# Performance work log

Measured on AMD Instinct MI355X. Metric: run time of the kernel, lower is better.

Reference implementation:

```python
import jax, jax.numpy as jnp
import numpy as np


def _lstm_cell(x, h, c, w_ih, w_hh, b_ih, b_hh):
    # PyTorch LSTMCell gate order: i, f, g, o
    z = x @ w_ih.T + h @ w_hh.T + b_ih + b_hh
    i, f, g, o = jnp.split(z, 4, axis=-1)
    c_new = jax.nn.sigmoid(f) * c + jax.nn.sigmoid(i) * jnp.tanh(g)
    h_new = jax.nn.sigmoid(o) * jnp.tanh(c_new)
    return h_new, c_new


def setup_inputs() -> dict:
    B, T_in, T_out = 32, 512, 512
    n_mel, n_frames = 80, 1
    n_enc, n_att, n_filt, K = 512, 128, 32, 31
    n_arnn, n_drnn, n_pre = 1024, 1024, 256
    keys = jax.random.split(jax.random.key(0), 25)
    r = lambda k, *s: jax.random.normal(keys[k], s, dtype=jnp.float32) * 0.05
    return {
        "memory": jax.random.normal(keys[0], (B, T_in, n_enc), dtype=jnp.float32),
        "decoder_inputs": jax.random.normal(keys[1], (B, n_mel, T_out), dtype=jnp.float32),
        "memory_lengths": jax.random.randint(keys[2], (B,), T_in // 2, T_in + 1).astype(jnp.int32),
        "prenet_w1": r(3, n_pre, n_mel * n_frames),
        "prenet_w2": r(4, n_pre, n_pre),
        "arnn_w_ih": r(5, 4 * n_arnn, n_pre + n_enc),
        "arnn_w_hh": r(6, 4 * n_arnn, n_arnn),
        "arnn_b_ih": r(7, 4 * n_arnn),
        "arnn_b_hh": r(8, 4 * n_arnn),
        "query_w": r(9, n_att, n_arnn),
        "memory_w": r(10, n_att, n_enc),
        "v_w": r(11, 1, n_att),
        "loc_conv_w": r(12, n_filt, 2, K),
        "loc_dense_w": r(13, n_att, n_filt),
        "drnn_w_ih": r(14, 4 * n_drnn, n_arnn + n_enc),
        "drnn_w_hh": r(15, 4 * n_drnn, n_drnn),
        "drnn_b_ih": r(16, 4 * n_drnn),
        "drnn_b_hh": r(17, 4 * n_drnn),
        "proj_w": r(18, n_mel * n_frames, n_drnn + n_enc),
        "proj_b": r(19, n_mel * n_frames),
        "gate_w": r(20, 1, n_drnn + n_enc),
        "gate_b": r(21, 1),
    }


def reference(memory, decoder_inputs, memory_lengths, prenet_w1, prenet_w2,
              arnn_w_ih, arnn_w_hh, arnn_b_ih, arnn_b_hh,
              query_w, memory_w, v_w, loc_conv_w, loc_dense_w,
              drnn_w_ih, drnn_w_hh, drnn_b_ih, drnn_b_hh,
              proj_w, proj_b, gate_w, gate_b):
    B, T_in, n_enc = memory.shape
    n_mel, T_out = decoder_inputs.shape[1], decoder_inputs.shape[2]
    n_arnn = arnn_w_hh.shape[1]
    n_drnn = drnn_w_hh.shape[1]
    K = loc_conv_w.shape[-1]
    dt = memory.dtype

    # mask: True = padded position (masked_fill with -inf in torch)
    mask = jnp.arange(T_in)[None, :] >= memory_lengths[:, None]          # (B, T_in)
    processed_memory = memory @ memory_w.T                               # (B, T_in, n_att)

    # teacher-forced inputs with go frame: (T_out+1, B, n_mel)
    go = jnp.zeros((1, B, n_mel), dt)
    dec_in = jnp.concatenate([go, jnp.transpose(decoder_inputs, (2, 0, 1))], 0)
    # prenet (dropout omitted for a deterministic reference)
    pre = jax.nn.relu(dec_in @ prenet_w1.T)
    pre = jax.nn.relu(pre @ prenet_w2.T)[:-1]                            # (T_out, B, n_pre)

    init = (jnp.zeros((B, n_arnn), dt), jnp.zeros((B, n_arnn), dt),
            jnp.zeros((B, n_drnn), dt), jnp.zeros((B, n_drnn), dt),
            jnp.zeros((B, T_in), dt), jnp.zeros((B, T_in), dt),
            jnp.zeros((B, n_enc), dt))

    def step(carry, pre_t):
        ah, ac, dh, dc, aw, aw_cum, actx = carry
        # attention RNN
        ah, ac = _lstm_cell(jnp.concatenate([pre_t, actx], -1), ah, ac,
                            arnn_w_ih, arnn_w_hh, arnn_b_ih, arnn_b_hh)
        # location-sensitive attention
        aw_cat = jnp.stack([aw, aw_cum], axis=1)                         # (B, 2, T_in)
        loc = jax.lax.conv_general_dilated(
            aw_cat, loc_conv_w, (1,), [(K // 2, K // 2)],
            dimension_numbers=("NCH", "OIH", "NCH"))                   # (B, n_filt, T_in)
        loc = jnp.transpose(loc, (0, 2, 1)) @ loc_dense_w.T              # (B, T_in, n_att)
        pq = (ah @ query_w.T)[:, None, :]                                # (B, 1, n_att)
        e = (jnp.tanh(pq + loc + processed_memory) @ v_w.T)[..., 0]      # (B, T_in)
        e = jnp.where(mask, -jnp.inf, e)
        aw = jax.nn.softmax(e, axis=1)
        actx = jnp.einsum("bt,bte->be", aw, memory)                      # (B, n_enc)
        aw_cum = aw_cum + aw
        # decoder RNN
        dh, dc = _lstm_cell(jnp.concatenate([ah, actx], -1), dh, dc,
                            drnn_w_ih, drnn_w_hh, drnn_b_ih, drnn_b_hh)
        dhc = jnp.concatenate([dh, actx], -1)
        mel = dhc @ proj_w.T + proj_b
        gate = (dhc @ gate_w.T + gate_b)[:, 0]
        return (ah, ac, dh, dc, aw, aw_cum, actx), (mel, gate, aw)

    _, (mels, gates, aligns) = jax.lax.scan(step, init, pre)
    mel_outputs = jnp.transpose(mels, (1, 2, 0))        # (B, n_mel, T_out)
    gate_outputs = gates.T                              # (B, T_out)
    alignments = jnp.transpose(aligns, (1, 0, 2))       # (B, T_out, T_in)
    return mel_outputs, gate_outputs, alignments
```

## Files before the change

kernel.cpp:

```cpp
#include <hip/hip_runtime.h>
#include <math.h>

#define NB 32
#define TIN 512
#define TOUT 512
#define NENC 512
#define NATT 128
#define NU 1024
#define NG 4096
#define NPRE 256
#define NMEL 80

#define WS_AH    0u
#define WS_AC    32768u
#define WS_DH    65536u
#define WS_DC    98304u
#define WS_ACTX  131072u
#define WS_AW    147456u
#define WS_AWCUM 163840u
#define WS_E     180224u
#define WS_PQ    196608u
#define WS_FLG   200704u
#define WS_ZD    201728u
#define WS_ZA    2823168u
#define WS_PM    4658176u
#define WS_PRE   6755328u
#define WS_WBF   10957824u
#define WS_STATE_ZERO_BYTES (WS_ZD * 4u)
#define OUT_ALIGN ((size_t)NB * NMEL * TOUT + (size_t)NB * TOUT)

#define BW_DIH 0u
#define BW_DHH 6291456u
#define BW_AIH 10485760u
#define BW_AHH 13631488u

__device__ __forceinline__ float fsigm(float x) { return 1.f / (1.f + __expf(-x)); }
__device__ __forceinline__ float ftanh(float x) { return 1.f - 2.f / (__expf(2.f * x) + 1.f); }
__device__ __forceinline__ float bf2f(unsigned short h) { return __uint_as_float((unsigned)h << 16); }

__device__ __forceinline__ void st_wt(float* p, float v) {
    asm volatile("global_store_dword %0, %1, off sc0 sc1" :: "v"(p), "v"(v) : "memory");
}

__global__ __launch_bounds__(256) void packbf_kernel(const float* __restrict__ src,
                                                     unsigned short* __restrict__ dst, int n) {
    for (int i = blockIdx.x * 256 + threadIdx.x; i < n; i += gridDim.x * 256) {
        unsigned u = __float_as_uint(src[i]);
        dst[i] = (unsigned short)((u + 0x7FFFu + ((u >> 16) & 1u)) >> 16);
    }
}

__global__ __launch_bounds__(256) void prenet1_kernel(const float* __restrict__ dec,
                                                      const float* __restrict__ w1,
                                                      float* __restrict__ pre) {
    int t = blockIdx.x;
    __shared__ float xl[NB][NMEL];
    for (int i = threadIdx.x; i < NB * NMEL; i += 256) {
        int b = i / NMEL, m = i % NMEL;
        xl[b][m] = (t == 0) ? 0.0f : dec[(b * NMEL + m) * TOUT + (t - 1)];
    }
    __syncthreads();
    int j = threadIdx.x;
    float acc[NB];
#pragma unroll
    for (int b = 0; b < NB; b++) acc[b] = 0.0f;
    for (int m = 0; m < NMEL; m++) {
        float w = w1[j * NMEL + m];
#pragma unroll
        for (int b = 0; b < NB; b++) acc[b] += xl[b][m] * w;
    }
    for (int b = 0; b < NB; b++) pre[((size_t)t * NB + b) * NPRE + j] = fmaxf(acc[b], 0.0f);
}

__global__ __launch_bounds__(256) void prenet2_kernel(const float* __restrict__ w2,
                                                      float* __restrict__ pre) {
    int t = blockIdx.x;
    __shared__ float hl[NB][NPRE];
    for (int i = threadIdx.x; i < NB * NPRE; i += 256)
        hl[i / NPRE][i % NPRE] = pre[(size_t)t * NB * NPRE + i];
    __syncthreads();
    int j = threadIdx.x;
    float acc[NB];
#pragma unroll
    for (int b = 0; b < NB; b++) acc[b] = 0.0f;
    for (int k = 0; k < NPRE; k++) {
        float w = w2[j * NPRE + k];
#pragma unroll
        for (int b = 0; b < NB; b++) acc[b] += hl[b][k] * w;
    }
    for (int b = 0; b < NB; b++) pre[((size_t)t * NB + b) * NPRE + j] = fmaxf(acc[b], 0.0f);
}

__global__ __launch_bounds__(128) void pm_kernel(const float* __restrict__ mem,
                                                 const float* __restrict__ mw,
                                                 float* __restrict__ pm) {
    int b = blockIdx.y, t0 = blockIdx.x * 4;
    __shared__ float ml[4][NENC];
    for (int i = threadIdx.x; i < 4 * NENC; i += 128)
        ml[i / NENC][i % NENC] = mem[((size_t)b * TIN + t0 + i / NENC) * NENC + (i % NENC)];
    __syncthreads();
    int a = threadIdx.x;
    float acc[4] = {0, 0, 0, 0};
    for (int e = 0; e < NENC; e++) {
        float w = mw[a * NENC + e];
#pragma unroll
        for (int tt = 0; tt < 4; tt++) acc[tt] += ml[tt][e] * w;
    }
    for (int tt = 0; tt < 4; tt++)
        pm[((size_t)b * TIN + t0 + tt) * NATT + a] = acc[tt];
}

__global__ __launch_bounds__(256) void z_all_kernel(
        const unsigned short* __restrict__ wbf,
        const float* __restrict__ ws_base, const float* __restrict__ pre_t,
        float* __restrict__ zd, float* __restrict__ za) {
    int col = blockIdx.x * 256 + threadIdx.x;
    int s = blockIdx.y;
    const float* ah   = ws_base + WS_AH;
    const float* dh   = ws_base + WS_DH;
    const float* actx = ws_base + WS_ACTX;
    const unsigned short* W; const float* x; int xs;
    if (s < 8)       { W = wbf + BW_DIH + (size_t)col * 1536 + s * 128;              x = ah + s * 128;           xs = NU;   }
    else if (s < 12) { W = wbf + BW_DIH + (size_t)col * 1536 + 1024 + (s - 8) * 128; x = actx + (s - 8) * 128;   xs = NENC; }
    else if (s < 20) { W = wbf + BW_DHH + (size_t)col * 1024 + (s - 12) * 128;       x = dh + (s - 12) * 128;    xs = NU;   }
    else if (s < 22) { W = wbf + BW_AIH + (size_t)col * 768 + (s - 20) * 128;        x = pre_t + (s - 20) * 128; xs = NPRE; }
    else if (s < 26) { W = wbf + BW_AIH + (size_t)col * 768 + 256 + (s - 22) * 128;  x = actx + (s - 22) * 128;  xs = NENC; }
    else             { W = wbf + BW_AHH + (size_t)col * 1024 + (s - 26) * 128;       x = ah + (s - 26) * 128;    xs = NU;   }

    float acc[NB];
#pragma unroll
    for (int b = 0; b < NB; b++) acc[b] = 0.0f;
    for (int k4 = 0; k4 < 32; k4++) {
        ushort4 h4 = *(const ushort4*)(W + k4 * 4);
        float w0 = bf2f(h4.x), w1 = bf2f(h4.y), w2 = bf2f(h4.z), w3 = bf2f(h4.w);
#pragma unroll
        for (int b = 0; b < NB; b++) {
            float4 x4 = *(const float4*)(x + (size_t)b * xs + k4 * 4);
            acc[b] = fmaf(w0, x4.x, acc[b]);
            acc[b] = fmaf(w1, x4.y, acc[b]);
            acc[b] = fmaf(w2, x4.z, acc[b]);
            acc[b] = fmaf(w3, x4.w, acc[b]);
        }
    }
    float* zp = ((s < 20) ? (zd + (size_t)s * NB * NG) : (za + (size_t)(s - 20) * NB * NG)) + col;
#pragma unroll
    for (int b = 0; b < NB; b++) zp[(size_t)b * NG] = acc[b];
}

__global__ __launch_bounds__(256) void softmax_ctx_kernel(const float* __restrict__ mem,
                                                          const float* __restrict__ E,
                                                          float* __restrict__ AW,
                                                          float* __restrict__ AWCUM,
                                                          float* __restrict__ ACTX,
                                                          float* __restrict__ out_align, int step) {
    int b = blockIdx.y, ec = blockIdx.x;
    __shared__ float el[TIN];
    __shared__ float red[256];
    __shared__ float part[4][64];
    const float* Eb = E + b * TIN;
    for (int i = threadIdx.x; i < TIN; i += 256) el[i] = Eb[i];
    __syncthreads();
    red[threadIdx.x] = fmaxf(el[threadIdx.x], el[threadIdx.x + 256]);
    __syncthreads();
    for (int s = 128; s > 0; s >>= 1) {
        if (threadIdx.x < s) red[threadIdx.x] = fmaxf(red[threadIdx.x], red[threadIdx.x + s]);
        __syncthreads();
    }
    float mx = red[0];
    __syncthreads();
    float p0 = __expf(el[threadIdx.x] - mx), p1 = __expf(el[threadIdx.x + 256] - mx);
    el[threadIdx.x] = p0; el[threadIdx.x + 256] = p1;
    red[threadIdx.x] = p0 + p1;
    __syncthreads();
    for (int s = 128; s > 0; s >>= 1) {
        if (threadIdx.x < s) red[threadIdx.x] += red[threadIdx.x + s];
        __syncthreads();
    }
    float inv = 1.0f / red[0];
    int ei = ec * 64 + (threadIdx.x & 63), tp4 = threadIdx.x >> 6;
    float acc = 0.0f;
    const float* mb = mem + (size_t)b * TIN * NENC + ei;
    for (int t = tp4 * 128; t < tp4 * 128 + 128; t++) acc += el[t] * mb[(size_t)t * NENC];
    part[tp4][threadIdx.x & 63] = acc;
    __syncthreads();
    if (threadIdx.x < 64) {
        float ctx = (part[0][threadIdx.x] + part[1][threadIdx.x] +
                     part[2][threadIdx.x] + part[3][threadIdx.x]) * inv;
        ACTX[b * NENC + ec * 64 + threadIdx.x] = ctx;
    }
    if (ec == 0) {
        for (int i = threadIdx.x; i < TIN; i += 256) {
            float a_ = el[i] * inv;
            AW[b * TIN + i] = a_;
            AWCUM[b * TIN + i] += a_;
            out_align[((size_t)b * TOUT + step) * TIN + i] = a_;
        }
    }
}

__global__ __launch_bounds__(512) void ge_kernel(
        const float* __restrict__ abih, const float* __restrict__ abhh,
        const float* __restrict__ qw,
        const float* __restrict__ dbih, const float* __restrict__ dbhh,
        const float* __restrict__ pjw, const float* __restrict__ pjb,
        const float* __restrict__ gtw, const float* __restrict__ gtb,
        const float* __restrict__ wc, const float* __restrict__ ldw,
        const float* __restrict__ vw, const int* __restrict__ mlen,
        float* __restrict__ ws, float* __restrict__ out, int t) {
    __shared__ float sm[5888];
    int tid = threadIdx.x, bid = blockIdx.x;
    unsigned* flg = (unsigned*)(ws + WS_FLG) + (t + 1);

    if (bid < 32) {
        if (t < 0) return;
        int b = bid;
        float* DH = ws + WS_DH + (size_t)b * NU;
        float* DC = ws + WS_DC + (size_t)b * NU;
        for (int u = tid; u < NU; u += 512) {
            float zi = dbih[u]          + dbhh[u];
            float zf = dbih[NU + u]     + dbhh[NU + u];
            float zg = dbih[2 * NU + u] + dbhh[2 * NU + u];
            float zo = dbih[3 * NU + u] + dbhh[3 * NU + u];
            for (int s = 0; s < 20; s++) {
                const float* z = ws + WS_ZD + ((size_t)s * NB + b) * NG;
                zi += z[u]; zf += z[NU + u]; zg += z[2 * NU + u]; zo += z[3 * NU + u];
            }
            float c = fsigm(zf) * DC[u] + fsigm(zi) * ftanh(zg);
            float h = fsigm(zo) * ftanh(c);
            DC[u] = c; DH[u] = h; sm[u] = h;
        }
        for (int i = tid; i < NENC; i += 512) sm[NU + i] = ws[WS_ACTX + b * NENC + i];
        __syncthreads();
        int col = tid >> 2, q = tid & 3;
        if (col < 81) {
            const float* wr = (col < 80) ? (pjw + (size_t)col * 1536) : gtw;
            const float* d4 = sm + q * 384;
            const float* w4 = wr + q * 384;
            float s = 0.f;
#pragma unroll
            for (int k4 = 0; k4 < 96; k4++) {
                float4 hv = *(const float4*)(d4 + k4 * 4);
                float4 wv = *(const float4*)(w4 + k4 * 4);
                s = fmaf(hv.x, wv.x, s); s = fmaf(hv.y, wv.y, s);
                s = fmaf(hv.z, wv.z, s); s = fmaf(hv.w, wv.w, s);
            }
            s += __shfl_xor(s, 1); s += __shfl_xor(s, 2);
            if (q == 0) {
                s += (col < 80) ? pjb[col] : gtb[0];
                if (col < 80) out[((size_t)b * NMEL + col) * TOUT + t] = s;
                else          out[(size_t)NB * NMEL * TOUT + (size_t)b * TOUT + t] = s;
            }
        }
        return;
    }
    if (bid < 64) {
        if (t + 1 >= TOUT) return;
        int b = bid - 32;
        float* AH = ws + WS_AH + (size_t)b * NU;
        float* AC = ws + WS_AC + (size_t)b * NU;
        for (int u = tid; u < NU; u += 512) {
            float zi = abih[u]          + abhh[u];
            float zf = abih[NU + u]     + abhh[NU + u];
            float zg = abih[2 * NU + u] + abhh[2 * NU + u];
            float zo = abih[3 * NU + u] + abhh[3 * NU + u];
            for (int s = 0; s < 14; s++) {
                const float* z = ws + WS_ZA + ((size_t)s * NB + b) * NG;
                zi += z[u]; zf += z[NU + u]; zg += z[2 * NU + u]; zo += z[3 * NU + u];
            }
            float c = fsigm(zf) * AC[u] + fsigm(zi) * ftanh(zg);
            float h = fsigm(zo) * ftanh(c);
            AC[u] = c; AH[u] = h; sm[u] = h;
        }
        __syncthreads();
        int a = tid >> 2, q = tid & 3;
        const float* qr = qw + (size_t)a * NU + q * 256;
        const float* h4 = sm + q * 256;
        float s = 0.f;
#pragma unroll
        for (int k4 = 0; k4 < 64; k4++) {
            float4 hv = *(const float4*)(h4 + k4 * 4);
            float4 wv = *(const float4*)(qr + k4 * 4);
            s = fmaf(hv.x, wv.x, s); s = fmaf(hv.y, wv.y, s);
            s = fmaf(hv.z, wv.z, s); s = fmaf(hv.w, wv.w, s);
        }
        s += __shfl_xor(s, 1); s += __shfl_xor(s, 2);
        if (q == 0) st_wt(&ws[WS_PQ + b * NATT + a], s);
        __syncthreads();
        if (tid == 0)
            __hip_atomic_fetch_add(flg, 1u, __ATOMIC_RELAXED, __HIP_MEMORY_SCOPE_AGENT);
        return;
    }
    if (t + 1 >= TOUT) return;
    int eb = bid - 64;
    int b = eb >> 2, tc = eb & 3;
    int tt = tid & 127, sub = tid >> 7;
    int tp_ = tc * 128 + tt;
    float* awl  = sm;
    float* cuml = sm + 512;
    float* locl = sm + 1024;
    float* pql  = sm + 5248;
    float* ep   = sm + 5376;
    for (int i = tid; i < TIN; i += 512) {
        awl[i]  = ws[WS_AW + b * TIN + i];
        cuml[i] = ws[WS_AWCUM + b * TIN + i];
    }
    if (tid == 0) {
        while (__hip_atomic_fetch_add(flg, 0u, __ATOMIC_RELAXED, __HIP_MEMORY_SCOPE_AGENT) < 32u)
            __builtin_amdgcn_s_sleep(8);
    }
    __syncthreads();
    if (tid < NATT)
        pql[tid] = __hip_atomic_load(&ws[WS_PQ + b * NATT + tid],
                                     __ATOMIC_RELAXED, __HIP_MEMORY_SCOPE_AGENT);
    __syncthreads();
    {
        int f0 = sub * 8;
        float sA[8];
#pragma unroll
        for (int j = 0; j < 8; ++j) sA[j] = 0.f;
        for (int d = 0; d < 31; ++d) {
            int tp = tp_ + d - 15;
            int tc_ = min(max(tp, 0), 511);
            bool ok = (tp >= 0) && (tp < 512);
            float a_ = ok ? awl[tc_] : 0.f;
            float c_ = ok ? cuml[tc_] : 0.f;
#pragma unroll
            for (int j = 0; j < 8; ++j)
                sA[j] = fmaf(a_, wc[(f0 + j) * 62 + d], fmaf(c_, wc[(f0 + j) * 62 + 31 + d], sA[j]));
        }
#pragma unroll
        for (int j = 0; j < 8; ++j) locl[tt * 33 + f0 + j] = sA[j];
    }
    __syncthreads();
    {
        float acc = 0.0f;
        const float* pmb = ws + WS_PM + ((size_t)b * TIN + tp_) * NATT;
        for (int a = sub * 32; a < sub * 32 + 32; a++) {
            float s_ = pql[a] + pmb[a];
            const float* lw = ldw + a * 32;
#pragma unroll
            for (int f = 0; f < 32; f++) s_ += locl[tt * 33 + f] * lw[f];
            acc += tanhf(s_) * vw[a];
        }
        ep[tt * 4 + sub] = acc;
    }
    __syncthreads();
    if (sub == 0) {
        float ev = ep[tt * 4] + ep[tt * 4 + 1] + ep[tt * 4 + 2] + ep[tt * 4 + 3];
        if (tp_ >= mlen[b]) ev = -3.0e38f;
        ws[WS_E + b * TIN + tp_] = ev;
    }
}

extern "C" void kernel_launch(void* const* d_in, const int* in_sizes, int n_in,
                              void* d_out, int out_size, void* d_ws, size_t ws_size,
                              hipStream_t stream) {
    const float* memory = (const float*)d_in[0];
    const float* dec    = (const float*)d_in[1];
    const int*   mlen   = (const int*)d_in[2];
    const float* pw1    = (const float*)d_in[3];
    const float* pw2    = (const float*)d_in[4];
    const float* awih   = (const float*)d_in[5];
    const float* awhh   = (const float*)d_in[6];
    const float* abih   = (const float*)d_in[7];
    const float* abhh   = (const float*)d_in[8];
    const float* qw     = (const float*)d_in[9];
    const float* mw     = (const float*)d_in[10];
    const float* vw     = (const float*)d_in[11];
    const float* wc     = (const float*)d_in[12];
    const float* ldw    = (const float*)d_in[13];
    const float* dwih   = (const float*)d_in[14];
    const float* dwhh   = (const float*)d_in[15];
    const float* dbih   = (const float*)d_in[16];
    const float* dbhh   = (const float*)d_in[17];
    const float* pjw    = (const float*)d_in[18];
    const float* pjb    = (const float*)d_in[19];
    const float* gtw    = (const float*)d_in[20];
    const float* gtb    = (const float*)d_in[21];
    float* ws  = (float*)d_ws;
    float* out = (float*)d_out;
    float* out_align = out + OUT_ALIGN;
    unsigned short* wbf = (unsigned short*)(ws + WS_WBF);

    hipMemsetAsync(ws, 0, WS_STATE_ZERO_BYTES, stream);
    hipMemsetAsync(ws + WS_PRE + (size_t)512 * NB * NPRE, 0, (size_t)NB * NPRE * 4, stream);

    packbf_kernel<<<1024, 256, 0, stream>>>(dwih, wbf + BW_DIH, 4096 * 1536);
    packbf_kernel<<<1024, 256, 0, stream>>>(dwhh, wbf + BW_DHH, 4096 * 1024);
    packbf_kernel<<<1024, 256, 0, stream>>>(awih, wbf + BW_AIH, 4096 * 768);
    packbf_kernel<<<1024, 256, 0, stream>>>(awhh, wbf + BW_AHH, 4096 * 1024);

    prenet1_kernel<<<TOUT, 256, 0, stream>>>(dec, pw1, ws + WS_PRE);
    prenet2_kernel<<<TOUT, 256, 0, stream>>>(pw2, ws + WS_PRE);
    pm_kernel<<<dim3(TIN / 4, NB), 128, 0, stream>>>(memory, mw, ws + WS_PM);

    z_all_kernel<<<dim3(16, 34), 256, 0, stream>>>(
        wbf, ws, ws + WS_PRE, ws + WS_ZD, ws + WS_ZA);
    ge_kernel<<<192, 512, 0, stream>>>(abih, abhh, qw, dbih, dbhh, pjw, pjb,
                                       gtw, gtb, wc, ldw, vw, mlen, ws, out, -1);

    for (int t = 0; t < TOUT; ++t) {
        softmax_ctx_kernel<<<dim3(8, NB), 256, 0, stream>>>(
            memory, ws + WS_E, ws + WS_AW, ws + WS_AWCUM, ws + WS_ACTX, out_align, t);
        z_all_kernel<<<dim3(16, 34), 256, 0, stream>>>(
            wbf, ws, ws + WS_PRE + (size_t)(t + 1) * NB * NPRE, ws + WS_ZD, ws + WS_ZA);
        ge_kernel<<<192, 512, 0, stream>>>(abih, abhh, qw, dbih, dbhh, pjw, pjb,
                                           gtw, gtb, wc, ldw, vw, mlen, ws, out, t);
    }
}
```

Before: 85.30 ms.

## Fuse softmax-context and gate-projection kernels with flag-based intra-kernel dependency

Merges the per-step softmax/attention-context kernel and the z projection kernel into one launch. Blocks computing z slices that do not depend on the attention context start at once. The 256 softmax blocks bump an atomic counter when done, and the context-dependent z slices spin on that counter before running. This removes one kernel launch per decoder step and overlaps the independent GEMV work with the softmax. The cost is spin-wait blocks that could deadlock if the softmax blocks are not scheduled first.

```diff
diff --git a/kernel.cpp b/kernel.cpp
--- a/kernel.cpp
+++ b/kernel.cpp
@@ -110,12 +110,10 @@
         pm[((size_t)b * TIN + t0 + tt) * NATT + a] = acc[tt];
 }
 
-__global__ __launch_bounds__(256) void z_all_kernel(
+__device__ __forceinline__ void z_slice_body(
         const unsigned short* __restrict__ wbf,
         const float* __restrict__ ws_base, const float* __restrict__ pre_t,
-        float* __restrict__ zd, float* __restrict__ za) {
-    int col = blockIdx.x * 256 + threadIdx.x;
-    int s = blockIdx.y;
+        float* __restrict__ zd, float* __restrict__ za, int s, int col) {
     const float* ah   = ws_base + WS_AH;
     const float* dh   = ws_base + WS_DH;
     const float* actx = ws_base + WS_ACTX;
@@ -147,55 +145,84 @@
     for (int b = 0; b < NB; b++) zp[(size_t)b * NG] = acc[b];
 }
 
-__global__ __launch_bounds__(256) void softmax_ctx_kernel(const float* __restrict__ mem,
-                                                          const float* __restrict__ E,
-                                                          float* __restrict__ AW,
-                                                          float* __restrict__ AWCUM,
-                                                          float* __restrict__ ACTX,
-                                                          float* __restrict__ out_align, int step) {
-    int b = blockIdx.y, ec = blockIdx.x;
-    __shared__ float el[TIN];
-    __shared__ float red[256];
-    __shared__ float part[4][64];
-    const float* Eb = E + b * TIN;
-    for (int i = threadIdx.x; i < TIN; i += 256) el[i] = Eb[i];
-    __syncthreads();
-    red[threadIdx.x] = fmaxf(el[threadIdx.x], el[threadIdx.x + 256]);
-    __syncthreads();
-    for (int s = 128; s > 0; s >>= 1) {
-        if (threadIdx.x < s) red[threadIdx.x] = fmaxf(red[threadIdx.x], red[threadIdx.x + s]);
-        __syncthreads();
-    }
-    float mx = red[0];
-    __syncthreads();
-    float p0 = __expf(el[threadIdx.x] - mx), p1 = __expf(el[threadIdx.x + 256] - mx);
-    el[threadIdx.x] = p0; el[threadIdx.x + 256] = p1;
-    red[threadIdx.x] = p0 + p1;
-    __syncthreads();
-    for (int s = 128; s > 0; s >>= 1) {
-        if (threadIdx.x < s) red[threadIdx.x] += red[threadIdx.x + s];
-        __syncthreads();
-    }
-    float inv = 1.0f / red[0];
-    int ei = ec * 64 + (threadIdx.x & 63), tp4 = threadIdx.x >> 6;
-    float acc = 0.0f;
-    const float* mb = mem + (size_t)b * TIN * NENC + ei;
-    for (int t = tp4 * 128; t < tp4 * 128 + 128; t++) acc += el[t] * mb[(size_t)t * NENC];
-    part[tp4][threadIdx.x & 63] = acc;
-    __syncthreads();
-    if (threadIdx.x < 64) {
-        float ctx = (part[0][threadIdx.x] + part[1][threadIdx.x] +
-                     part[2][threadIdx.x] + part[3][threadIdx.x]) * inv;
-        ACTX[b * NENC + ec * 64 + threadIdx.x] = ctx;
-    }
-    if (ec == 0) {
-        for (int i = threadIdx.x; i < TIN; i += 256) {
-            float a_ = el[i] * inv;
-            AW[b * TIN + i] = a_;
-            AWCUM[b * TIN + i] += a_;
-            out_align[((size_t)b * TOUT + step) * TIN + i] = a_;
-        }
-    }
+__global__ __launch_bounds__(256) void z_all_kernel(
+        const unsigned short* __restrict__ wbf,
+        const float* __restrict__ ws_base, const float* __restrict__ pre_t,
+        float* __restrict__ zd, float* __restrict__ za) {
+    z_slice_body(wbf, ws_base, pre_t, zd, za, (int)blockIdx.y,
+                 (int)blockIdx.x * 256 + (int)threadIdx.x);
+}
+
+__global__ __launch_bounds__(256) void zs_kernel(
+        const unsigned short* __restrict__ wbf, const float* __restrict__ memory,
+        float* __restrict__ ws, float* __restrict__ out_align,
+        const float* __restrict__ pre_t1, int t) {
+    __shared__ float sm[1024];
+    int tid = threadIdx.x, bid = blockIdx.x;
+    unsigned* flg = (unsigned*)(ws + WS_FLG) + 512 + t;
+
+    if (bid < 416) {
+        int sidx = bid >> 4;
+        int s = sidx < 8 ? sidx : (sidx < 18 ? sidx + 4 : sidx + 8);
+        z_slice_body(wbf, ws, pre_t1, ws + WS_ZD, ws + WS_ZA, s, (bid & 15) * 256 + tid);
+        return;
+    }
+    if (bid < 672) {
+        int smb = bid - 416;
+        int b = smb >> 3, ec = smb & 7;
+        float* el = sm; float* red = sm + 512; float* part = sm + 768;
+        const float* Eb = ws + WS_E + b * TIN;
+        for (int i = tid; i < TIN; i += 256) el[i] = Eb[i];
+        __syncthreads();
+        red[tid] = fmaxf(el[tid], el[tid + 256]);
+        __syncthreads();
+        for (int s = 128; s > 0; s >>= 1) {
+            if (tid < s) red[tid] = fmaxf(red[tid], red[tid + s]);
+            __syncthreads();
+        }
+        float mx = red[0];
+        __syncthreads();
+        float p0 = __expf(el[tid] - mx), p1 = __expf(el[tid + 256] - mx);
+        el[tid] = p0; el[tid + 256] = p1;
+        red[tid] = p0 + p1;
+        __syncthreads();
+        for (int s = 128; s > 0; s >>= 1) {
+            if (tid < s) red[tid] += red[tid + s];
+            __syncthreads();
+        }
+        float inv = 1.0f / red[0];
+        int ei = ec * 64 + (tid & 63), tp4 = tid >> 6;
+        float acc = 0.0f;
+        const float* mb = memory + (size_t)b * TIN * NENC + ei;
+        for (int u = tp4 * 128; u < tp4 * 128 + 128; u++) acc += el[u] * mb[(size_t)u * NENC];
+        part[tp4 * 64 + (tid & 63)] = acc;
+        __syncthreads();
+        if (tid < 64) {
+            float ctx = (part[tid] + part[64 + tid] + part[128 + tid] + part[192 + tid]) * inv;
+            st_wt(&ws[WS_ACTX + b * NENC + ec * 64 + tid], ctx);
+        }
+        if (ec == 0) {
+            for (int i = tid; i < TIN; i += 256) {
+                float a_ = el[i] * inv;
+                ws[WS_AW + b * TIN + i] = a_;
+                ws[WS_AWCUM + b * TIN + i] += a_;
+                out_align[((size_t)b * TOUT + t) * TIN + i] = a_;
+            }
+        }
+        __syncthreads();
+        if (tid == 0)
+            __hip_atomic_fetch_add(flg, 1u, __ATOMIC_RELAXED, __HIP_MEMORY_SCOPE_AGENT);
+        return;
+    }
+    int zb = bid - 672;
+    int sidx = zb >> 4;
+    int s = (sidx < 4) ? 8 + sidx : 18 + sidx;
+    if (tid == 0) {
+        while (__hip_atomic_fetch_add(flg, 0u, __ATOMIC_RELAXED, __HIP_MEMORY_SCOPE_AGENT) < 256u)
+            __builtin_amdgcn_s_sleep(8);
+    }
+    __syncthreads();
+    z_slice_body(wbf, ws, pre_t1, ws + WS_ZD, ws + WS_ZA, s, (zb & 15) * 256 + tid);
 }
 
 __global__ __launch_bounds__(512) void ge_kernel(
@@ -400,10 +427,9 @@
                                        gtw, gtb, wc, ldw, vw, mlen, ws, out, -1);
 
     for (int t = 0; t < TOUT; ++t) {
-        softmax_ctx_kernel<<<dim3(8, NB), 256, 0, stream>>>(
-            memory, ws + WS_E, ws + WS_AW, ws + WS_AWCUM, ws + WS_ACTX, out_align, t);
-        z_all_kernel<<<dim3(16, 34), 256, 0, stream>>>(
-            wbf, ws, ws + WS_PRE + (size_t)(t + 1) * NB * NPRE, ws + WS_ZD, ws + WS_ZA);
+        zs_kernel<<<800, 256, 0, stream>>>(
+            wbf, memory, ws, out_align,
+            ws + WS_PRE + (size_t)(t + 1) * NB * NPRE, t);
         ge_kernel<<<192, 512, 0, stream>>>(abih, abhh, qw, dbih, dbhh, pjw, pjb,
                                            gtw, gtb, wc, ldw, vw, mlen, ws, out, t);
     }
```

After: 112.7 ms. +32.1%, slower.
